# Kernel optimization log

Measured on AMD Instinct MI355X. Metric: run time of the kernel, lower is better.

The kernel has to match this reference:

```python
import jax, jax.numpy as jnp
import numpy as np
from jax.scipy.special import logsumexp

N, T, C, H, V = 8, 512, 1024, 256, 32000


def _res_layer(x, W1, b1, W2, b2):
    # hmm-lm ResLayer: x + ReLU(Linear(ReLU(Linear(x))))
    return x + jax.nn.relu(jax.nn.relu(x @ W1.T + b1) @ W2.T + b2)


def setup_inputs() -> dict:
    key = jax.random.key(0)
    ks = jax.random.split(key, 12)
    g = lambda k, shape: jax.random.normal(k, shape, jnp.float32) * (1.0 / np.sqrt(shape[-1]))
    return {
        "text": jax.random.randint(ks[0], (N, T), 0, V),
        "start_emb": jax.random.normal(ks[1], (H,), jnp.float32),
        "start_lin_W": g(ks[2], (H, H)),
        "start_lin_b": jnp.zeros((H,), jnp.float32),
        "start_res_W1": g(ks[3], (2, H, H)),
        "start_res_b1": jnp.zeros((2, H), jnp.float32),
        "start_res_W2": g(ks[4], (2, H, H)),
        "start_res_b2": jnp.zeros((2, H), jnp.float32),
        "state_emb": g(ks[5], (C, H)),
        "next_state_emb": g(ks[6], (C, H)),
        "preterminal_emb": g(ks[7], (C, H)),
        "term_res_W1": g(ks[8], (2, H, H)),
        "term_res_b1": jnp.zeros((2, H), jnp.float32),
        "term_res_W2": g(ks[9], (2, H, H)),
        "term_res_b2": jnp.zeros((2, H), jnp.float32),
        "terminal_emb": g(ks[10], (V, H)),
    }


def reference(text, start_emb, start_lin_W, start_lin_b,
              start_res_W1, start_res_b1, start_res_W2, start_res_b2,
              state_emb, next_state_emb, preterminal_emb,
              term_res_W1, term_res_b1, term_res_W2, term_res_b2,
              terminal_emb):
    # --- start distribution: start_mlp(start_emb) @ next_state_emb.T (tie_start) ---
    fx = start_emb @ start_lin_W.T + start_lin_b
    for i in range(2):
        fx = _res_layer(fx, start_res_W1[i], start_res_b1[i], start_res_W2[i], start_res_b2[i])
    start = jax.nn.log_softmax(fx @ next_state_emb.T)            # [C]

    # --- transition: log_softmax(state_emb @ next_state_emb.T) ---
    transition = jax.nn.log_softmax(state_emb @ next_state_emb.T, axis=-1)  # [C, C]

    # --- emission: log_softmax(terminal_mlp(preterminal_emb) @ terminal_emb.T) ---
    ft = preterminal_emb
    for i in range(2):
        ft = _res_layer(ft, term_res_W1[i], term_res_b1[i], term_res_W2[i], term_res_b2[i])
    emission = jax.nn.log_softmax(ft @ terminal_emb.T, axis=-1)  # [C, V]
    emis_t = emission.T                                          # [V, C]

    # --- HMM forward (log-space) scan; evidence = logsumexp(alpha_T) summed over batch ---
    alpha0 = start[None, :] + emis_t[text[:, 0]]                 # [N, C]

    def step(alpha, x_t):
        # alpha: [N, C]; x_t: [N]
        a = logsumexp(alpha[:, :, None] + transition[None], axis=1) + emis_t[x_t]
        return a, None

    alpha_T, _ = jax.lax.scan(step, alpha0, text[:, 1:].T)       # time-major [T-1, N]
    evidence = logsumexp(alpha_T, axis=-1).sum()
    return evidence
```

## Files before the change

kernel.cpp:

```cpp
#include <hip/hip_runtime.h>
#include <stdint.h>
#include <stddef.h>

#define N_ 8
#define T_ 512
#define C_ 1024
#define H_ 256
#define V_ 32000

#define OFF_START   0u
#define OFF_LSE     4096u
#define OFF_EVP     8192u
#define OFF_FT      81920u
#define OFF_P       1130496u
#define OFF_PART    5324800u
#define OFF_EEXP    5849088u
#define OFF_BUF     22626304u
#define OFF_CNT     22724608u
#define OFF_PT      22725120u

typedef __attribute__((ext_vector_type(8))) short short8;
typedef __attribute__((ext_vector_type(4))) float floatx4;

__device__ __forceinline__ float dot4(float4 a, float4 b) {
  return a.x*b.x + a.y*b.y + a.z*b.z + a.w*b.w;
}

__device__ __forceinline__ unsigned short f2bf(float f) {
  unsigned u = __float_as_uint(f);
  unsigned r = u + 0x7fffu + ((u >> 16) & 1u);
  return (unsigned short)(r >> 16);
}

__device__ __forceinline__ unsigned pk_bf2(float x, float y) {
  return ((unsigned)f2bf(y) << 16) | (unsigned)f2bf(x);
}

__device__ __forceinline__ short8 pack8(float4 a, float4 b) {
  union { short8 s; unsigned u[4]; } r;
  r.u[0] = pk_bf2(a.x, a.y);
  r.u[1] = pk_bf2(a.z, a.w);
  r.u[2] = pk_bf2(b.x, b.y);
  r.u[3] = pk_bf2(b.z, b.w);
  return r.s;
}

__global__ __launch_bounds__(256) void k_start(
    const float* __restrict__ se, const float* __restrict__ lw, const float* __restrict__ lb,
    const float* __restrict__ W1, const float* __restrict__ b1,
    const float* __restrict__ W2, const float* __restrict__ b2,
    const float* __restrict__ nse, float* __restrict__ out_start)
{
  __shared__ float xs[H_], fx[H_], h1[H_];
  __shared__ float lg[C_];
  __shared__ float redk[4];
  int tid = threadIdx.x;
  xs[tid] = se[tid];
  __syncthreads();
  {
    float acc = lb[tid];
    const float4* wr = (const float4*)(lw + (size_t)tid*H_);
    for (int k = 0; k < H_/4; ++k) acc += dot4(wr[k], *(const float4*)&xs[k*4]);
    fx[tid] = acc;
  }
  __syncthreads();
  for (int L = 0; L < 2; ++L) {
    {
      float acc = b1[L*H_ + tid];
      const float4* wr = (const float4*)(W1 + (size_t)(L*H_ + tid)*H_);
      for (int k = 0; k < H_/4; ++k) acc += dot4(wr[k], *(const float4*)&fx[k*4]);
      h1[tid] = fmaxf(acc, 0.f);
    }
    __syncthreads();
    {
      float acc = b2[L*H_ + tid];
      const float4* wr = (const float4*)(W2 + (size_t)(L*H_ + tid)*H_);
      for (int k = 0; k < H_/4; ++k) acc += dot4(wr[k], *(const float4*)&h1[k*4]);
      fx[tid] += fmaxf(acc, 0.f);
    }
    __syncthreads();
  }
  float lmax = -1e30f;
  for (int r = 0; r < 4; ++r) {
    int cc = tid + r*256;
    float acc = 0.f;
    const float4* er = (const float4*)(nse + (size_t)cc*H_);
    for (int k = 0; k < H_/4; ++k) acc += dot4(er[k], *(const float4*)&fx[k*4]);
    lg[cc] = acc;
    lmax = fmaxf(lmax, acc);
  }
  for (int m = 32; m; m >>= 1) lmax = fmaxf(lmax, __shfl_xor(lmax, m, 64));
  if ((tid & 63) == 0) redk[tid >> 6] = lmax;
  __syncthreads();
  float M = fmaxf(fmaxf(redk[0], redk[1]), fmaxf(redk[2], redk[3]));
  __syncthreads();
  float ssum = 0.f;
  for (int r = 0; r < 4; ++r) ssum += __expf(lg[tid + r*256] - M);
  for (int m = 32; m; m >>= 1) ssum += __shfl_xor(ssum, m, 64);
  if ((tid & 63) == 0) redk[tid >> 6] = ssum;
  __syncthreads();
  float S = redk[0] + redk[1] + redk[2] + redk[3];
  float lse = M + __logf(S);
  for (int r = 0; r < 4; ++r) {
    int cc = tid + r*256;
    out_start[cc] = lg[cc] - lse;
  }
}

__global__ __launch_bounds__(256) void k_gemm_cc(
    const float* __restrict__ A, const float* __restrict__ B, float* __restrict__ Cout)
{
  __shared__ float As[64][69];
  __shared__ float Bs[64][69];
  int tid = threadIdx.x;
  int bi = blockIdx.y, bj = blockIdx.x;
  int sr = tid >> 2, sq = tid & 3;
  int tx = tid & 15, ty = tid >> 4;
  float acc[4][4] = {};
  for (int kb = 0; kb < H_; kb += 64) {
    __syncthreads();
    {
      const float* ar = A + (size_t)(bi*64 + sr)*H_ + kb + sq*16;
      const float* br = B + (size_t)(bj*64 + sr)*H_ + kb + sq*16;
#pragma unroll
      for (int qq = 0; qq < 4; ++qq) {
        float4 av = *(const float4*)(ar + qq*4);
        float4 bv = *(const float4*)(br + qq*4);
        int kk = sq*16 + qq*4;
        As[sr][kk+0]=av.x; As[sr][kk+1]=av.y; As[sr][kk+2]=av.z; As[sr][kk+3]=av.w;
        Bs[sr][kk+0]=bv.x; Bs[sr][kk+1]=bv.y; Bs[sr][kk+2]=bv.z; Bs[sr][kk+3]=bv.w;
      }
    }
    __syncthreads();
#pragma unroll 4
    for (int k = 0; k < 64; ++k) {
      float a0 = As[ty*4+0][k], a1 = As[ty*4+1][k], a2 = As[ty*4+2][k], a3 = As[ty*4+3][k];
      float b0 = Bs[tx*4+0][k], b1 = Bs[tx*4+1][k], b2 = Bs[tx*4+2][k], b3 = Bs[tx*4+3][k];
      acc[0][0]+=a0*b0; acc[0][1]+=a0*b1; acc[0][2]+=a0*b2; acc[0][3]+=a0*b3;
      acc[1][0]+=a1*b0; acc[1][1]+=a1*b1; acc[1][2]+=a1*b2; acc[1][3]+=a1*b3;
      acc[2][0]+=a2*b0; acc[2][1]+=a2*b1; acc[2][2]+=a2*b2; acc[2][3]+=a2*b3;
      acc[3][0]+=a3*b0; acc[3][1]+=a3*b1; acc[3][2]+=a3*b2; acc[3][3]+=a3*b3;
    }
  }
#pragma unroll
  for (int ii = 0; ii < 4; ++ii)
#pragma unroll
    for (int jj = 0; jj < 4; ++jj)
      Cout[(size_t)(bi*64 + ty*4 + ii)*C_ + bj*64 + tx*4 + jj] = acc[ii][jj];
}

__global__ __launch_bounds__(256) void k_softmax_rows(float* __restrict__ P)
{
  __shared__ float redk[4];
  int row = blockIdx.x, tid = threadIdx.x;
  float4* pr = (float4*)(P + (size_t)row*C_);
  float4 v = pr[tid];
  float m = fmaxf(fmaxf(v.x, v.y), fmaxf(v.z, v.w));
  for (int mm = 32; mm; mm >>= 1) m = fmaxf(m, __shfl_xor(m, mm, 64));
  if ((tid & 63) == 0) redk[tid >> 6] = m;
  __syncthreads();
  float M = fmaxf(fmaxf(redk[0], redk[1]), fmaxf(redk[2], redk[3]));
  __syncthreads();
  float4 e;
  e.x = __expf(v.x - M); e.y = __expf(v.y - M); e.z = __expf(v.z - M); e.w = __expf(v.w - M);
  float s = e.x + e.y + e.z + e.w;
  for (int mm = 32; mm; mm >>= 1) s += __shfl_xor(s, mm, 64);
  if ((tid & 63) == 0) redk[tid >> 6] = s;
  __syncthreads();
  float S = redk[0] + redk[1] + redk[2] + redk[3];
  float inv = 1.0f / S;
  e.x *= inv; e.y *= inv; e.z *= inv; e.w *= inv;
  pr[tid] = e;
}

__global__ __launch_bounds__(256) void k_packT(
    const float* __restrict__ P, unsigned short* __restrict__ PT)
{
  __shared__ float ts[64][68];
  int tid = threadIdx.x;
  int bi = blockIdx.y, bj = blockIdx.x;
  int rl = tid >> 4;
  int cl4 = (tid & 15) * 4;
#pragma unroll
  for (int rr = 0; rr < 4; ++rr) {
    int row = rr*16 + rl;
    float4 v = *(const float4*)(P + (size_t)(bi*64 + row)*C_ + bj*64 + cl4);
    ts[row][cl4+0]=v.x; ts[row][cl4+1]=v.y; ts[row][cl4+2]=v.z; ts[row][cl4+3]=v.w;
  }
  __syncthreads();
  int jl = tid >> 2;
  int m0 = (tid & 3) * 16;
  unsigned pk[8];
#pragma unroll
  for (int u = 0; u < 8; ++u)
    pk[u] = pk_bf2(ts[m0 + u*2][jl], ts[m0 + u*2 + 1][jl]);
  char* dst = (char*)(PT + (size_t)(bj*64 + jl)*1024 + bi*64 + m0);
  *(uint4*)(dst +  0) = *(const uint4*)&pk[0];
  *(uint4*)(dst + 16) = *(const uint4*)&pk[4];
}

__global__ __launch_bounds__(256) void k_mlp(
    const float* __restrict__ inp, const float* __restrict__ W1, const float* __restrict__ b1,
    const float* __restrict__ W2, const float* __restrict__ b2, float* __restrict__ ft)
{
  __shared__ float xs[4][H_];
  __shared__ float hs[4][H_];
  int tid = threadIdx.x;
  int r0 = blockIdx.x * 4;
  int lr = tid >> 6, lc = (tid & 63) * 4;
  *(float4*)&xs[lr][lc] = *(const float4*)(inp + (size_t)(r0+lr)*H_ + lc);
  __syncthreads();
  for (int L = 0; L < 2; ++L) {
    {
      const float4* wr = (const float4*)(W1 + (size_t)(L*H_ + tid)*H_);
      float bb = b1[L*H_ + tid];
      float a0=bb, a1=bb, a2=bb, a3=bb;
      for (int k = 0; k < H_/4; ++k) {
        float4 w = wr[k];
        a0 += dot4(w, *(const float4*)&xs[0][k*4]);
        a1 += dot4(w, *(const float4*)&xs[1][k*4]);
        a2 += dot4(w, *(const float4*)&xs[2][k*4]);
        a3 += dot4(w, *(const float4*)&xs[3][k*4]);
      }
      hs[0][tid]=fmaxf(a0,0.f); hs[1][tid]=fmaxf(a1,0.f);
      hs[2][tid]=fmaxf(a2,0.f); hs[3][tid]=fmaxf(a3,0.f);
    }
    __syncthreads();
    {
      const float4* wr = (const float4*)(W2 + (size_t)(L*H_ + tid)*H_);
      float bb = b2[L*H_ + tid];
      float a0=bb, a1=bb, a2=bb, a3=bb;
      for (int k = 0; k < H_/4; ++k) {
        float4 w = wr[k];
        a0 += dot4(w, *(const float4*)&hs[0][k*4]);
        a1 += dot4(w, *(const float4*)&hs[1][k*4]);
        a2 += dot4(w, *(const float4*)&hs[2][k*4]);
        a3 += dot4(w, *(const float4*)&hs[3][k*4]);
      }
      xs[0][tid] += fmaxf(a0,0.f); xs[1][tid] += fmaxf(a1,0.f);
      xs[2][tid] += fmaxf(a2,0.f); xs[3][tid] += fmaxf(a3,0.f);
    }
    __syncthreads();
  }
  *(float4*)(ft + (size_t)(r0+lr)*H_ + lc) = *(float4*)&xs[lr][lc];
}

#define LSE_VSPLIT 16
#define LSE_VPB    2000
#define LSE_CHUNKS 125

__global__ __launch_bounds__(256) void k_lse_mfma(
    const float* __restrict__ ft, const float* __restrict__ emb, float* __restrict__ part)
{
  int tid = threadIdx.x;
  int lane = tid & 63;
  int w = tid >> 6;
  int q = blockIdx.x;
  int jb = blockIdx.y * 64 + w * 16;
  int r16 = lane & 15, kb = lane >> 4;

  short8 A[8];
  {
    const float* arow = ft + (size_t)(jb + r16) * H_ + kb * 8;
#pragma unroll
    for (int ks = 0; ks < 8; ++ks) {
      float4 a = *(const float4*)(arow + ks * 32);
      float4 b = *(const float4*)(arow + ks * 32 + 4);
      A[ks] = pack8(a, b);
    }
  }
  float s0 = 0.f, s1 = 0.f, s2 = 0.f, s3 = 0.f;
  const float* embq = emb + (size_t)q * LSE_VPB * H_;
#pragma unroll 1
  for (int ch = 0; ch < LSE_CHUNKS; ++ch) {
    const float* brow = embq + (size_t)(ch * 16 + r16) * H_ + kb * 8;
    floatx4 acca = {0,0,0,0}, accb = {0,0,0,0};
#pragma unroll
    for (int ks = 0; ks < 8; ks += 2) {
      float4 x0 = *(const float4*)(brow + ks * 32);
      float4 y0 = *(const float4*)(brow + ks * 32 + 4);
      float4 x1 = *(const float4*)(brow + ks * 32 + 32);
      float4 y1 = *(const float4*)(brow + ks * 32 + 36);
      acca = __builtin_amdgcn_mfma_f32_16x16x32_bf16(A[ks],   pack8(x0, y0), acca, 0, 0, 0);
      accb = __builtin_amdgcn_mfma_f32_16x16x32_bf16(A[ks+1], pack8(x1, y1), accb, 0, 0, 0);
    }
    s0 += __expf(acca[0] + accb[0]);
    s1 += __expf(acca[1] + accb[1]);
    s2 += __expf(acca[2] + accb[2]);
    s3 += __expf(acca[3] + accb[3]);
  }
#pragma unroll
  for (int mm = 1; mm <= 8; mm <<= 1) {
    s0 += __shfl_xor(s0, mm, 64);
    s1 += __shfl_xor(s1, mm, 64);
    s2 += __shfl_xor(s2, mm, 64);
    s3 += __shfl_xor(s3, mm, 64);
  }
  if (r16 == 0) {
    int jrow = jb + kb * 4;
    part[(size_t)(jrow + 0) * LSE_VSPLIT + q] = s0;
    part[(size_t)(jrow + 1) * LSE_VSPLIT + q] = s1;
    part[(size_t)(jrow + 2) * LSE_VSPLIT + q] = s2;
    part[(size_t)(jrow + 3) * LSE_VSPLIT + q] = s3;
  }
}

__global__ __launch_bounds__(256) void k_lse_reduce(
    const float* __restrict__ part, float* __restrict__ lse_row)
{
  int row = blockIdx.x * 256 + threadIdx.x;
  const float4* p = (const float4*)(part + (size_t)row * LSE_VSPLIT);
  float4 a = p[0], b = p[1], c = p[2], d = p[3];
  float s = a.x+a.y+a.z+a.w + b.x+b.y+b.z+b.w + c.x+c.y+c.z+c.w + d.x+d.y+d.z+d.w;
  lse_row[row] = __logf(s);
}

__global__ __launch_bounds__(256) void k_eexp_mfma(
    const float* __restrict__ ft, const float* __restrict__ emb, const int* __restrict__ text,
    const float* __restrict__ lse_row, float* __restrict__ EEXP)
{
  int tid = threadIdx.x;
  int lane = tid & 63;
  int w = tid >> 6;
  int jb = blockIdx.y * 64 + w * 16;
  int tb = blockIdx.x * 64;
  int r16 = lane & 15, kb = lane >> 4;

  short8 A[8];
  {
    const float* arow = ft + (size_t)(jb + r16) * H_ + kb * 8;
#pragma unroll
    for (int ks = 0; ks < 8; ++ks) {
      float4 a = *(const float4*)(arow + ks * 32);
      float4 b = *(const float4*)(arow + ks * 32 + 4);
      A[ks] = pack8(a, b);
    }
  }
  float4 lsej = *(const float4*)(lse_row + jb + kb * 4);

#pragma unroll 1
  for (int tc = 0; tc < 4; ++tc) {
    int idx = tb + tc * 16 + r16;
    int tok = text[idx];
    const float* brow = emb + (size_t)tok * H_ + kb * 8;
    floatx4 acca = {0,0,0,0}, accb = {0,0,0,0};
#pragma unroll
    for (int ks = 0; ks < 8; ks += 2) {
      float4 x0 = *(const float4*)(brow + ks * 32);
      float4 y0 = *(const float4*)(brow + ks * 32 + 4);
      float4 x1 = *(const float4*)(brow + ks * 32 + 32);
      float4 y1 = *(const float4*)(brow + ks * 32 + 36);
      acca = __builtin_amdgcn_mfma_f32_16x16x32_bf16(A[ks],   pack8(x0, y0), acca, 0, 0, 0);
      accb = __builtin_amdgcn_mfma_f32_16x16x32_bf16(A[ks+1], pack8(x1, y1), accb, 0, 0, 0);
    }
    float4 o;
    o.x = __expf(acca[0] + accb[0] - lsej.x);
    o.y = __expf(acca[1] + accb[1] - lsej.y);
    o.z = __expf(acca[2] + accb[2] - lsej.z);
    o.w = __expf(acca[3] + accb[3] - lsej.w);
    *(float4*)(EEXP + (size_t)idx * C_ + jb + kb * 4) = o;
  }
}

#define SCAN_LDS (131072 + 4096 + 256 + 32)

__global__ __launch_bounds__(256) void k_scan(
    const unsigned short* __restrict__ PT, const float* __restrict__ EEXP,
    const float* __restrict__ startv,
    float* __restrict__ bufG, unsigned* __restrict__ cntG, float* __restrict__ evp)
{
  extern __shared__ char smem[];
  char*  Pl   = smem;
  char*  Al   = smem + 131072;
  char*  Ub   = smem + 135168;
  float* redm = (float*)(smem + 135424);

  int tid  = threadIdx.x;
  int bid  = blockIdx.x;
  int c    = bid >> 2;
  int ng   = bid & 3;
  int n0   = ng * 2;
  int lane = tid & 63;
  int w    = tid >> 6;
  int s    = tid >> 7;
  int k0   = (tid & 127) * 8;
  int r16  = lane & 15;
  int kb4  = lane >> 4;

  unsigned* cnt = cntG + ng * 16;
  float* bufq[3];
  bufq[0] = bufG + (size_t)(0*4 + ng)*2048;
  bufq[1] = bufG + (size_t)(1*4 + ng)*2048;
  bufq[2] = bufG + (size_t)(2*4 + ng)*2048;

  {
    int col = tid & 63, q = tid >> 6;
    const char* src = (const char*)(PT + (size_t)(c*64 + col)*1024) + q*512;
    char* dstb = Pl + (size_t)col*2048;
    int swz = (col & 15) << 4;
#pragma unroll
    for (int u = 0; u < 32; ++u)
      *(uint4*)(dstb + ((q*512 + u*16) ^ swz)) = *(const uint4*)(src + u*16);
  }

  short8 vb[16][2];
#pragma unroll
  for (int i = 0; i < 16; ++i)
#pragma unroll
    for (int q = 0; q < 2; ++q)
      vb[i][q] = *(const short8*)((const char*)PT +
          ((size_t)((w*16 + i)*16 + r16)*1024 + c*64 + q*32 + kb4*8)*2);

  __syncthreads();

  float ls   = 0.f;
  float Muse = 1.f;
  int s2   = r16 & 1;
  int ucol = c*64 + w*16 + r16;

#pragma unroll 1
  for (int r = 0; r < 256; ++r) {
    float ue0 = 0.f, ue1 = 0.f;
    if (lane < 16) {
      ue0 = EEXP[((size_t)(n0+0)*T_ + (2*r+1))*C_ + ucol];
      ue1 = EEXP[((size_t)(n0+1)*T_ + (2*r+1))*C_ + ucol];
    }
    float4 e0 = *(const float4*)(EEXP + ((size_t)(n0+s)*T_ + 2*r)*C_ + k0);
    float4 e1 = *(const float4*)(EEXP + ((size_t)(n0+s)*T_ + 2*r)*C_ + k0 + 4);

    float av[8];
    if (r == 0) {
      av[0] = __expf(startv[k0+0]) * e0.x;
      av[1] = __expf(startv[k0+1]) * e0.y;
      av[2] = __expf(startv[k0+2]) * e0.z;
      av[3] = __expf(startv[k0+3]) * e0.w;
      av[4] = __expf(startv[k0+4]) * e1.x;
      av[5] = __expf(startv[k0+5]) * e1.y;
      av[6] = __expf(startv[k0+6]) * e1.z;
      av[7] = __expf(startv[k0+7]) * e1.w;
    } else {
      unsigned tgt = 64u * (unsigned)r;
      int guard = 0;
      for (;;) {
        unsigned f = __hip_atomic_load(cnt, __ATOMIC_RELAXED, __HIP_MEMORY_SCOPE_AGENT);
        if (f >= tgt) break;
        __builtin_amdgcn_s_sleep(1);
        if (++guard > 4000000) break;
      }
      float* srcb = bufq[(r-1)%3] + s*1024 + k0;
      float sv[8];
#pragma unroll
      for (int j = 0; j < 8; ++j)
        sv[j] = __hip_atomic_load(srcb + j, __ATOMIC_RELAXED, __HIP_MEMORY_SCOPE_AGENT);
      av[0]=sv[0]*e0.x; av[1]=sv[1]*e0.y; av[2]=sv[2]*e0.z; av[3]=sv[3]*e0.w;
      av[4]=sv[4]*e1.x; av[5]=sv[5]*e1.y; av[6]=sv[6]*e1.z; av[7]=sv[7]*e1.w;
    }

    ls += __logf(Muse);
    float rinv = 1.0f / Muse;
    float m8 = fmaxf(fmaxf(fmaxf(av[0],av[1]),fmaxf(av[2],av[3])),
                     fmaxf(fmaxf(av[4],av[5]),fmaxf(av[6],av[7])));
#pragma unroll
    for (int mm = 1; mm <= 32; mm <<= 1) m8 = fmaxf(m8, __shfl_xor(m8, mm, 64));
    if (lane == 0) redm[w] = m8;
    {
      unsigned pk[4];
      pk[0] = pk_bf2(av[0]*rinv, av[1]*rinv);
      pk[1] = pk_bf2(av[2]*rinv, av[3]*rinv);
      pk[2] = pk_bf2(av[4]*rinv, av[5]*rinv);
      pk[3] = pk_bf2(av[6]*rinv, av[7]*rinv);
      int blk = k0 >> 5;
      *(uint4*)(Al + blk*128 + s*64 + (((k0&31)*2) ^ ((blk&3)<<4))) = *(const uint4*)pk;
    }
    if (r != 0 && tid < 128) {
      int ss = tid >> 6, col = c*64 + (tid & 63);
      __hip_atomic_store(bufq[(r+1)%3] + ss*1024 + col, 0.0f,
                         __ATOMIC_RELAXED, __HIP_MEMORY_SCOPE_AGENT);
    }
    __syncthreads();
    Muse = fmaxf(fmaxf(redm[0], redm[1]), fmaxf(redm[2], redm[3])) * rinv;

    floatx4 acc[4] = {{0,0,0,0},{0,0,0,0},{0,0,0,0},{0,0,0,0}};
    {
      const char* bcol = Pl + (size_t)(w*16 + r16)*2048;
      int swzc = r16 << 4;
#pragma unroll
      for (int ch = 0; ch < 4; ++ch)
#pragma unroll
        for (int b8 = 0; b8 < 8; ++b8) {
          int blk = b8*4 + ch;
          short8 af = *(const short8*)(Al + blk*128 + s2*64 + ((kb4*16) ^ ((blk&3)<<4)));
          short8 bf = *(const short8*)(bcol + ((blk*64 + kb4*16) ^ swzc));
          acc[ch] = __builtin_amdgcn_mfma_f32_16x16x32_bf16(af, bf, acc[ch], 0, 0, 0);
        }
    }
    floatx4 us;
    us[0] = (acc[0][0]+acc[1][0]) + (acc[2][0]+acc[3][0]);
    us[1] = (acc[0][1]+acc[1][1]) + (acc[2][1]+acc[3][1]);

    if (r == 255) {
      if (lane < 16) {
        (void)__hip_atomic_fetch_add(bufq[0] + 0*1024 + ucol, us[0]*ue0,
                                     __ATOMIC_RELAXED, __HIP_MEMORY_SCOPE_AGENT);
        (void)__hip_atomic_fetch_add(bufq[0] + 1*1024 + ucol, us[1]*ue1,
                                     __ATOMIC_RELAXED, __HIP_MEMORY_SCOPE_AGENT);
      }
      asm volatile("s_waitcnt vmcnt(0)" ::: "memory");
      if (lane == 0)
        (void)__hip_atomic_fetch_add(cnt, 1u, __ATOMIC_RELAXED, __HIP_MEMORY_SCOPE_AGENT);
    } else {
      if (lane < 16) {
        *(unsigned short*)(Ub + 0*128 + (w*16 + r16)*2) = f2bf(us[0] * ue0);
        *(unsigned short*)(Ub + 1*128 + (w*16 + r16)*2) = f2bf(us[1] * ue1);
      }
      __syncthreads();
      short8 ua0 = *(const short8*)(Ub + s2*128 +  0 + kb4*16);
      short8 ua1 = *(const short8*)(Ub + s2*128 + 64 + kb4*16);
      float* bufp = bufq[r%3];
#pragma unroll
      for (int i = 0; i < 16; ++i) {
        floatx4 a = {0,0,0,0};
        a = __builtin_amdgcn_mfma_f32_16x16x32_bf16(ua0, vb[i][0], a, 0, 0, 0);
        a = __builtin_amdgcn_mfma_f32_16x16x32_bf16(ua1, vb[i][1], a, 0, 0, 0);
        if (lane < 16) {
          int jc = (w*16 + i)*16 + r16;
          (void)__hip_atomic_fetch_add(bufp + jc, a[0],
                                       __ATOMIC_RELAXED, __HIP_MEMORY_SCOPE_AGENT);
          (void)__hip_atomic_fetch_add(bufp + 1024 + jc, a[1],
                                       __ATOMIC_RELAXED, __HIP_MEMORY_SCOPE_AGENT);
        }
      }
      asm volatile("s_waitcnt vmcnt(0)" ::: "memory");
      if (lane == 0)
        (void)__hip_atomic_fetch_add(cnt, 1u, __ATOMIC_RELAXED, __HIP_MEMORY_SCOPE_AGENT);
    }
  }

  if (c == 0) {
    int guard = 0;
    for (;;) {
      unsigned f = __hip_atomic_load(cnt, __ATOMIC_RELAXED, __HIP_MEMORY_SCOPE_AGENT);
      if (f >= 16384u) break;
      __builtin_amdgcn_s_sleep(1);
      if (++guard > 4000000) break;
    }
    float* srcb = bufq[0] + s*1024 + k0;
    float ssum = 0.f;
#pragma unroll
    for (int j = 0; j < 8; ++j)
      ssum += __hip_atomic_load(srcb + j, __ATOMIC_RELAXED, __HIP_MEMORY_SCOPE_AGENT);
#pragma unroll
    for (int mm = 1; mm <= 32; mm <<= 1) ssum += __shfl_xor(ssum, mm, 64);
    if (lane == 0) redm[w] = ssum;
    __syncthreads();
    if (tid == 0)   evp[n0]     = ls + __logf(redm[0] + redm[1]);
    if (tid == 128) evp[n0 + 1] = ls + __logf(redm[2] + redm[3]);
  }
}

__global__ void k_final(const float* __restrict__ evp, float* __restrict__ out)
{
  if (threadIdx.x == 0) {
    float s = 0.f;
#pragma unroll
    for (int i = 0; i < N_; ++i) s += evp[i];
    out[0] = s;
  }
}

extern "C" void kernel_launch(void* const* d_in, const int* in_sizes, int n_in,
                              void* d_out, int out_size, void* d_ws, size_t ws_size,
                              hipStream_t stream)
{
  const int*   text      = (const int*)  d_in[0];
  const float* start_emb = (const float*)d_in[1];
  const float* slw       = (const float*)d_in[2];
  const float* slb       = (const float*)d_in[3];
  const float* sW1       = (const float*)d_in[4];
  const float* sb1       = (const float*)d_in[5];
  const float* sW2       = (const float*)d_in[6];
  const float* sb2       = (const float*)d_in[7];
  const float* state_emb = (const float*)d_in[8];
  const float* nse       = (const float*)d_in[9];
  const float* pre_emb   = (const float*)d_in[10];
  const float* tW1       = (const float*)d_in[11];
  const float* tb1       = (const float*)d_in[12];
  const float* tW2       = (const float*)d_in[13];
  const float* tb2       = (const float*)d_in[14];
  const float* term_emb  = (const float*)d_in[15];

  char* ws = (char*)d_ws;
  float*          w_start = (float*)         (ws + OFF_START);
  float*          w_lse   = (float*)         (ws + OFF_LSE);
  float*          w_evp   = (float*)         (ws + OFF_EVP);
  float*          w_ft    = (float*)         (ws + OFF_FT);
  float*          w_P     = (float*)         (ws + OFF_P);
  float*          w_part  = (float*)         (ws + OFF_PART);
  float*          w_eexp  = (float*)         (ws + OFF_EEXP);
  float*          w_buf   = (float*)         (ws + OFF_BUF);
  unsigned*       w_cnt   = (unsigned*)      (ws + OFF_CNT);
  unsigned short* w_pt    = (unsigned short*)(ws + OFF_PT);

  (void)hipMemsetAsync(ws + OFF_BUF, 0, 98304 + 512, stream);

  k_start<<<1, 256, 0, stream>>>(start_emb, slw, slb, sW1, sb1, sW2, sb2, nse, w_start);
  k_gemm_cc<<<dim3(16,16), 256, 0, stream>>>(state_emb, nse, w_P);
  k_softmax_rows<<<C_, 256, 0, stream>>>(w_P);
  k_packT<<<dim3(16,16), 256, 0, stream>>>(w_P, w_pt);
  k_mlp<<<C_/4, 256, 0, stream>>>(pre_emb, tW1, tb1, tW2, tb2, w_ft);
  k_lse_mfma<<<dim3(LSE_VSPLIT, 16), 256, 0, stream>>>(w_ft, term_emb, w_part);
  k_lse_reduce<<<4, 256, 0, stream>>>(w_part, w_lse);
  k_eexp_mfma<<<dim3(64, 16), 256, 0, stream>>>(w_ft, term_emb, text, w_lse, w_eexp);

  (void)hipFuncSetAttribute((const void*)k_scan, hipFuncAttributeMaxDynamicSharedMemorySize, SCAN_LDS);
  k_scan<<<64, 256, SCAN_LDS, stream>>>(w_pt, w_eexp, w_start, w_buf, w_cnt, w_evp);
  k_final<<<1, 64, 0, stream>>>(w_evp, (float*)d_out);
}
```

Baseline: 1.843 ms.

## Replace scan counter barrier with fixed-point tagged 64-bit atomic accumulators

The cross-block scan no longer uses a shared arrival counter plus a vmcnt drain before each step. Each partial sum is now added as a 64-bit fixed-point value whose top bits count the contributions. Consumers poll their own eight slots until the tag shows every producer has arrived, which removes the counter round trip and the store-drain wait. Normalisation now divides by the current step's per-sequence max before publishing, instead of carrying a lagged scale. This risks fixed-point precision and overflow, and every poll reads wider 64-bit data.

```diff
diff --git a/kernel.cpp b/kernel.cpp
--- a/kernel.cpp
+++ b/kernel.cpp
@@ -16,11 +16,14 @@
 #define OFF_PART    5324800u
 #define OFF_EEXP    5849088u
 #define OFF_BUF     22626304u
-#define OFF_CNT     22724608u
-#define OFF_PT      22725120u
+#define OFF_PT      22822912u
 
 typedef __attribute__((ext_vector_type(8))) short short8;
 typedef __attribute__((ext_vector_type(4))) float floatx4;
+
+#define FMASK ((1ull << 58) - 1ull)
+#define FSCALE 281474976710656.0f
+#define FINV   3.552713678800501e-15f
 
 __device__ __forceinline__ float dot4(float4 a, float4 b) {
   return a.x*b.x + a.y*b.y + a.z*b.z + a.w*b.w;
@@ -367,7 +370,7 @@
 __global__ __launch_bounds__(256) void k_scan(
     const unsigned short* __restrict__ PT, const float* __restrict__ EEXP,
     const float* __restrict__ startv,
-    float* __restrict__ bufG, unsigned* __restrict__ cntG, float* __restrict__ evp)
+    unsigned long long* __restrict__ bufG, float* __restrict__ evp)
 {
   extern __shared__ char smem[];
   char*  Pl   = smem;
@@ -387,8 +390,7 @@
   int r16  = lane & 15;
   int kb4  = lane >> 4;
 
-  unsigned* cnt = cntG + ng * 16;
-  float* bufq[3];
+  unsigned long long* bufq[3];
   bufq[0] = bufG + (size_t)(0*4 + ng)*2048;
   bufq[1] = bufG + (size_t)(1*4 + ng)*2048;
   bufq[2] = bufG + (size_t)(2*4 + ng)*2048;
@@ -413,8 +415,7 @@
 
   __syncthreads();
 
-  float ls   = 0.f;
-  float Muse = 1.f;
+  float ls0 = 0.f, ls1 = 0.f;
   int s2   = r16 & 1;
   int ucol = c*64 + w*16 + r16;
 
@@ -439,25 +440,32 @@
       av[6] = __expf(startv[k0+6]) * e1.z;
       av[7] = __expf(startv[k0+7]) * e1.w;
     } else {
-      unsigned tgt = 64u * (unsigned)r;
+      unsigned long long want = 16ull * (unsigned long long)(1 + ((r-1) & 1));
+      unsigned long long* srcb = bufq[(r-1)%3] + (size_t)s*1024 + k0;
+      unsigned long long vv[8];
       int guard = 0;
       for (;;) {
-        unsigned f = __hip_atomic_load(cnt, __ATOMIC_RELAXED, __HIP_MEMORY_SCOPE_AGENT);
-        if (f >= tgt) break;
+#pragma unroll
+        for (int j = 0; j < 8; ++j)
+          vv[j] = __hip_atomic_load(srcb + j, __ATOMIC_RELAXED, __HIP_MEMORY_SCOPE_AGENT);
+        bool ok = true;
+#pragma unroll
+        for (int j = 0; j < 8; ++j) ok &= ((vv[j] >> 58) == want);
+        if (ok) break;
         __builtin_amdgcn_s_sleep(1);
-        if (++guard > 4000000) break;
+        if (++guard > 2000000) break;
       }
-      float* srcb = bufq[(r-1)%3] + s*1024 + k0;
       float sv[8];
 #pragma unroll
       for (int j = 0; j < 8; ++j)
-        sv[j] = __hip_atomic_load(srcb + j, __ATOMIC_RELAXED, __HIP_MEMORY_SCOPE_AGENT);
+        sv[j] = (float)(vv[j] & FMASK) * FINV;
       av[0]=sv[0]*e0.x; av[1]=sv[1]*e0.y; av[2]=sv[2]*e0.z; av[3]=sv[3]*e0.w;
       av[4]=sv[4]*e1.x; av[5]=sv[5]*e1.y; av[6]=sv[6]*e1.z; av[7]=sv[7]*e1.w;
-    }
-
-    ls += __logf(Muse);
-    float rinv = 1.0f / Muse;
+      if (tid < 128)
+        __hip_atomic_store(bufq[(r+1)%3] + (size_t)c*128 + tid, 0ull,
+                           __ATOMIC_RELAXED, __HIP_MEMORY_SCOPE_AGENT);
+    }
+
     float m8 = fmaxf(fmaxf(fmaxf(av[0],av[1]),fmaxf(av[2],av[3])),
                      fmaxf(fmaxf(av[4],av[5]),fmaxf(av[6],av[7])));
 #pragma unroll
@@ -465,20 +473,19 @@
     if (lane == 0) redm[w] = m8;
     {
       unsigned pk[4];
-      pk[0] = pk_bf2(av[0]*rinv, av[1]*rinv);
-      pk[1] = pk_bf2(av[2]*rinv, av[3]*rinv);
-      pk[2] = pk_bf2(av[4]*rinv, av[5]*rinv);
-      pk[3] = pk_bf2(av[6]*rinv, av[7]*rinv);
+      pk[0] = pk_bf2(av[0], av[1]);
+      pk[1] = pk_bf2(av[2], av[3]);
+      pk[2] = pk_bf2(av[4], av[5]);
+      pk[3] = pk_bf2(av[6], av[7]);
       int blk = k0 >> 5;
       *(uint4*)(Al + blk*128 + s*64 + (((k0&31)*2) ^ ((blk&3)<<4))) = *(const uint4*)pk;
     }
-    if (r != 0 && tid < 128) {
-      int ss = tid >> 6, col = c*64 + (tid & 63);
-      __hip_atomic_store(bufq[(r+1)%3] + ss*1024 + col, 0.0f,
-                         __ATOMIC_RELAXED, __HIP_MEMORY_SCOPE_AGENT);
-    }
-    __syncthreads();
-    Muse = fmaxf(fmaxf(redm[0], redm[1]), fmaxf(redm[2], redm[3])) * rinv;
+    __syncthreads();
+    float M0 = fmaxf(redm[0], redm[1]);
+    float M1 = fmaxf(redm[2], redm[3]);
+    ls0 += __logf(M0);
+    ls1 += __logf(M1);
+    float iM0 = 1.0f / M0, iM1 = 1.0f / M1;
 
     floatx4 acc[4] = {{0,0,0,0},{0,0,0,0},{0,0,0,0},{0,0,0,0}};
     {
@@ -498,25 +505,26 @@
     us[0] = (acc[0][0]+acc[1][0]) + (acc[2][0]+acc[3][0]);
     us[1] = (acc[0][1]+acc[1][1]) + (acc[2][1]+acc[3][1]);
 
+    unsigned long long inc = (unsigned long long)(1 + (r & 1)) << 58;
+
     if (r == 255) {
       if (lane < 16) {
-        (void)__hip_atomic_fetch_add(bufq[0] + 0*1024 + ucol, us[0]*ue0,
+        unsigned long long f0 = (unsigned long long)(us[0]*ue0*iM0 * FSCALE) + inc;
+        unsigned long long f1 = (unsigned long long)(us[1]*ue1*iM1 * FSCALE) + inc;
+        (void)__hip_atomic_fetch_add(bufq[0] + 0*1024 + ucol, f0,
                                      __ATOMIC_RELAXED, __HIP_MEMORY_SCOPE_AGENT);
-        (void)__hip_atomic_fetch_add(bufq[0] + 1*1024 + ucol, us[1]*ue1,
+        (void)__hip_atomic_fetch_add(bufq[0] + 1*1024 + ucol, f1,
                                      __ATOMIC_RELAXED, __HIP_MEMORY_SCOPE_AGENT);
       }
-      asm volatile("s_waitcnt vmcnt(0)" ::: "memory");
-      if (lane == 0)
-        (void)__hip_atomic_fetch_add(cnt, 1u, __ATOMIC_RELAXED, __HIP_MEMORY_SCOPE_AGENT);
     } else {
       if (lane < 16) {
-        *(unsigned short*)(Ub + 0*128 + (w*16 + r16)*2) = f2bf(us[0] * ue0);
-        *(unsigned short*)(Ub + 1*128 + (w*16 + r16)*2) = f2bf(us[1] * ue1);
+        *(unsigned short*)(Ub + 0*128 + (w*16 + r16)*2) = f2bf(us[0] * ue0 * iM0);
+        *(unsigned short*)(Ub + 1*128 + (w*16 + r16)*2) = f2bf(us[1] * ue1 * iM1);
       }
       __syncthreads();
       short8 ua0 = *(const short8*)(Ub + s2*128 +  0 + kb4*16);
       short8 ua1 = *(const short8*)(Ub + s2*128 + 64 + kb4*16);
-      float* bufp = bufq[r%3];
+      unsigned long long* bufp = bufq[r%3];
 #pragma unroll
       for (int i = 0; i < 16; ++i) {
         floatx4 a = {0,0,0,0};
@@ -524,37 +532,42 @@
         a = __builtin_amdgcn_mfma_f32_16x16x32_bf16(ua1, vb[i][1], a, 0, 0, 0);
         if (lane < 16) {
           int jc = (w*16 + i)*16 + r16;
-          (void)__hip_atomic_fetch_add(bufp + jc, a[0],
+          unsigned long long f0 = (unsigned long long)(a[0] * FSCALE) + inc;
+          unsigned long long f1 = (unsigned long long)(a[1] * FSCALE) + inc;
+          (void)__hip_atomic_fetch_add(bufp + jc, f0,
                                        __ATOMIC_RELAXED, __HIP_MEMORY_SCOPE_AGENT);
-          (void)__hip_atomic_fetch_add(bufp + 1024 + jc, a[1],
+          (void)__hip_atomic_fetch_add(bufp + 1024 + jc, f1,
                                        __ATOMIC_RELAXED, __HIP_MEMORY_SCOPE_AGENT);
         }
       }
-      asm volatile("s_waitcnt vmcnt(0)" ::: "memory");
-      if (lane == 0)
-        (void)__hip_atomic_fetch_add(cnt, 1u, __ATOMIC_RELAXED, __HIP_MEMORY_SCOPE_AGENT);
     }
   }
 
   if (c == 0) {
+    unsigned long long* srcb = bufq[0] + (size_t)s*1024 + k0;
+    unsigned long long vv[8];
     int guard = 0;
     for (;;) {
-      unsigned f = __hip_atomic_load(cnt, __ATOMIC_RELAXED, __HIP_MEMORY_SCOPE_AGENT);
-      if (f >= 16384u) break;
+#pragma unroll
+      for (int j = 0; j < 8; ++j)
+        vv[j] = __hip_atomic_load(srcb + j, __ATOMIC_RELAXED, __HIP_MEMORY_SCOPE_AGENT);
+      bool ok = true;
+#pragma unroll
+      for (int j = 0; j < 8; ++j) ok &= ((vv[j] >> 58) == 2ull);
+      if (ok) break;
       __builtin_amdgcn_s_sleep(1);
       if (++guard > 4000000) break;
     }
-    float* srcb = bufq[0] + s*1024 + k0;
     float ssum = 0.f;
 #pragma unroll
     for (int j = 0; j < 8; ++j)
-      ssum += __hip_atomic_load(srcb + j, __ATOMIC_RELAXED, __HIP_MEMORY_SCOPE_AGENT);
+      ssum += (float)(vv[j] & FMASK) * FINV;
 #pragma unroll
     for (int mm = 1; mm <= 32; mm <<= 1) ssum += __shfl_xor(ssum, mm, 64);
     if (lane == 0) redm[w] = ssum;
     __syncthreads();
-    if (tid == 0)   evp[n0]     = ls + __logf(redm[0] + redm[1]);
-    if (tid == 128) evp[n0 + 1] = ls + __logf(redm[2] + redm[3]);
+    if (tid == 0)   evp[n0]     = ls0 + __logf(redm[0] + redm[1]);
+    if (tid == 128) evp[n0 + 1] = ls1 + __logf(redm[2] + redm[3]);
   }
 }
 
@@ -590,18 +603,17 @@
   const float* term_emb  = (const float*)d_in[15];
 
   char* ws = (char*)d_ws;
-  float*          w_start = (float*)         (ws + OFF_START);
-  float*          w_lse   = (float*)         (ws + OFF_LSE);
-  float*          w_evp   = (float*)         (ws + OFF_EVP);
-  float*          w_ft    = (float*)         (ws + OFF_FT);
-  float*          w_P     = (float*)         (ws + OFF_P);
-  float*          w_part  = (float*)         (ws + OFF_PART);
-  float*          w_eexp  = (float*)         (ws + OFF_EEXP);
-  float*          w_buf   = (float*)         (ws + OFF_BUF);
-  unsigned*       w_cnt   = (unsigned*)      (ws + OFF_CNT);
-  unsigned short* w_pt    = (unsigned short*)(ws + OFF_PT);
-
-  (void)hipMemsetAsync(ws + OFF_BUF, 0, 98304 + 512, stream);
+  float*              w_start = (float*)             (ws + OFF_START);
+  float*              w_lse   = (float*)             (ws + OFF_LSE);
+  float*              w_evp   = (float*)             (ws + OFF_EVP);
+  float*              w_ft    = (float*)             (ws + OFF_FT);
+  float*              w_P     = (float*)             (ws + OFF_P);
+  float*              w_part  = (float*)             (ws + OFF_PART);
+  float*              w_eexp  = (float*)             (ws + OFF_EEXP);
+  unsigned long long* w_buf   = (unsigned long long*)(ws + OFF_BUF);
+  unsigned short*     w_pt    = (unsigned short*)    (ws + OFF_PT);
+
+  (void)hipMemsetAsync(ws + OFF_BUF, 0, 196608, stream);
 
   k_start<<<1, 256, 0, stream>>>(start_emb, slw, slb, sW1, sb1, sW2, sb2, nse, w_start);
   k_gemm_cc<<<dim3(16,16), 256, 0, stream>>>(state_emb, nse, w_P);
@@ -613,6 +625,6 @@
   k_eexp_mfma<<<dim3(64, 16), 256, 0, stream>>>(w_ft, term_emb, text, w_lse, w_eexp);
 
   (void)hipFuncSetAttribute((const void*)k_scan, hipFuncAttributeMaxDynamicSharedMemorySize, SCAN_LDS);
-  k_scan<<<64, 256, SCAN_LDS, stream>>>(w_pt, w_eexp, w_start, w_buf, w_cnt, w_evp);
+  k_scan<<<64, 256, SCAN_LDS, stream>>>(w_pt, w_eexp, w_start, w_buf, w_evp);
   k_final<<<1, 64, 0, stream>>>(w_evp, (float*)d_out);
 }
```

New measurement: 1.779 ms. 3.4% less time.
